# Kernel optimization log

Hardware: AMD Instinct MI355X
Metric: run time of the kernel (lower is better)

The kernel has to match this reference:

```python
import jax, jax.numpy as jnp
import numpy as np

MUL = 64          # multiplicity of 0e and 1o channels
N_NODES = 50000
N_EDGES = 800000
NUM_NEIGHBORS = 16.0
SILU_NORM = 1.679177  # e3nn normalize2mom constant for silu


def setup_inputs() -> dict:
    key = jax.random.key(0)
    ks = jax.random.split(key, 9)
    node_in = jax.random.normal(ks[0], (N_NODES, 4 * MUL), dtype=jnp.float32)  # 64x0e + 64x1o
    edge_src = jax.random.randint(ks[1], (N_EDGES,), 0, N_NODES)
    edge_dst = jax.random.randint(ks[2], (N_EDGES,), 0, N_NODES)
    edge_attr = jax.random.normal(ks[3], (N_EDGES, 4), dtype=jnp.float32)      # 1x0e + 1x1o
    edge_len_emb = jax.random.uniform(ks[4], (N_EDGES, 10), dtype=jnp.float32)
    # tensor-product path weights [mul_in, mul_out] (mul_edge = 1)
    w_00_0 = jax.random.normal(ks[5], (MUL, MUL), dtype=jnp.float32)  # 0e x 0e -> 0e
    w_11_0 = jax.random.normal(ks[6], (MUL, MUL), dtype=jnp.float32)  # 1o x 1o -> 0e
    w_01_1 = jax.random.normal(ks[7], (MUL, MUL), dtype=jnp.float32)  # 0e x 1o -> 1o
    w_10_1 = jax.random.normal(ks[8], (MUL, MUL), dtype=jnp.float32)  # 1o x 0e -> 1o
    kf = jax.random.split(jax.random.fold_in(key, 1), 2)
    fc_w1 = jax.random.normal(kf[0], (10, 64), dtype=jnp.float32)
    fc_w2 = jax.random.normal(kf[1], (64, 1), dtype=jnp.float32)
    return {"node_in": node_in, "edge_attr": edge_attr, "edge_len_emb": edge_len_emb,
            "w_00_0": w_00_0, "w_11_0": w_11_0, "w_01_1": w_01_1, "w_10_1": w_10_1,
            "fc_w1": fc_w1, "fc_w2": fc_w2, "edge_src": edge_src, "edge_dst": edge_dst}


def reference(node_in, edge_attr, edge_len_emb, w_00_0, w_11_0, w_01_1, w_10_1,
              fc_w1, fc_w2, edge_src, edge_dst):
    # gather source node features per edge
    src = node_in[edge_src]                      # [E, 256]
    s0 = src[:, :MUL]                            # [E, mul]       scalars 0e
    s1 = src[:, MUL:].reshape(-1, MUL, 3)        # [E, mul, 3]    vectors 1o
    a0 = edge_attr[:, 0:1]                       # [E, 1]   edge 0e
    a1 = edge_attr[:, 1:4]                       # [E, 3]   edge 1o

    # fully-connected tensor product: path norm 1/sqrt(num_paths * fan_in)
    alpha = np.float32(1.0 / np.sqrt(2.0 * MUL))
    inv_sqrt3 = np.float32(1.0 / np.sqrt(3.0))
    # scalar output: 0e x 0e -> 0e  and  1o . 1o -> 0e (CG = delta/sqrt(3))
    out0 = alpha * (jnp.einsum('ei,io->eo', s0 * a0, w_00_0)
                    + inv_sqrt3 * jnp.einsum('eim,em,io->eo', s1, a1, w_11_0))   # [E, mul]
    # vector output: 0e x 1o -> 1o  and  1o x 0e -> 1o (CG = identity)
    out1 = alpha * (jnp.einsum('ei,io,em->eom', s0, w_01_1, a1)
                    + jnp.einsum('eim,io->eom', s1 * a0[:, :, None], w_10_1))     # [E, mul, 3]
    msg_ang = jnp.concatenate([out0, out1.reshape(-1, 3 * MUL)], axis=1)         # [E, 256]

    # radial MLP gate: FullyConnectedNet([10, 64, 1], silu)
    h = jax.nn.silu(edge_len_emb @ fc_w1 / np.float32(np.sqrt(10.0))) * np.float32(SILU_NORM)
    msg_rad = h @ fc_w2 / np.float32(np.sqrt(64.0))                              # [E, 1]

    messages = msg_ang * msg_rad
    agg = jax.ops.segment_sum(messages, edge_dst, num_segments=node_in.shape[0])
    return agg / np.float32(np.sqrt(NUM_NEIGHBORS))
```

## Files before the change

kernel.cpp:

```cpp
#include <hip/hip_runtime.h>

#define NE 800000
#define NN 50000
#define MAXD 56
#define FILL_BLK (NE / 256)
#define XC_BLK (NN / 8)

typedef __attribute__((ext_vector_type(4))) unsigned short ushort4v;
typedef __attribute__((ext_vector_type(8))) unsigned short ushort8;
typedef __attribute__((ext_vector_type(4))) _Float16 f16x4;
typedef __attribute__((ext_vector_type(4))) float f32x4;

static constexpr float ALPHA      = 0.08838834764831845f;
static constexpr float INV3       = 0.57735026918962576f;
static constexpr float INV_SQRT10 = 0.31622776601683794f;
static constexpr float SILU_NORM  = 1.679177f;
static constexpr float QSCALE     = ALPHA * 0.25f;

__device__ __forceinline__ unsigned short f2h_bits(float f) {
  _Float16 h = (_Float16)f;
  unsigned short b;
  __builtin_memcpy(&b, &h, 2);
  return b;
}
__device__ __forceinline__ float h2f_bits(unsigned int b) {
  unsigned short s = (unsigned short)b;
  _Float16 h;
  __builtin_memcpy(&h, &s, 2);
  return (float)h;
}
__device__ __forceinline__ unsigned int packh2(float lo, float hi) {
  return (unsigned int)f2h_bits(lo) | ((unsigned int)f2h_bits(hi) << 16);
}

__global__ __launch_bounds__(256) void k_combo(
    const float* __restrict__ X, unsigned short* __restrict__ Xp,
    const float* __restrict__ attr, const float* __restrict__ emb,
    const float* __restrict__ w1, const float* __restrict__ w2,
    const int* __restrict__ esrc, const int* __restrict__ edst,
    int* __restrict__ cur, uint4* __restrict__ ell) {
  __shared__ float lds[2816];
  if (blockIdx.x < FILL_BLK) {
    int eb = blockIdx.x * 256;
    int e = eb + threadIdx.x;
    int dst = edst[e];
    int src = esrc[e];
    float4 a = *(const float4*)(attr + (size_t)e * 4);
    int slot = atomicAdd(&cur[dst], 1);

    const float* ebase = emb + (size_t)eb * 10;
#pragma unroll
    for (int j = 0; j < 10; j++)
      lds[j * 256 + threadIdx.x] = ebase[j * 256 + threadIdx.x];
    __syncthreads();
    const float* x = lds + threadIdx.x * 10;
    float r = 0.f;
#pragma unroll
    for (int j = 0; j < 64; j++) {
      float d = 0.f;
#pragma unroll
      for (int k = 0; k < 10; k++) d = fmaf(x[k], w1[k * 64 + j], d);
      d *= INV_SQRT10;
      float h = d * __builtin_amdgcn_rcpf(1.f + __expf(-d)) * SILU_NORM;
      r = fmaf(h, w2[j], r);
    }
    r *= 0.125f * QSCALE;
    if (slot < MAXD) {
      ell[(size_t)dst * MAXD + slot] =
          make_uint4((unsigned)src, packh2(r * a.x, r * a.y),
                     packh2(r * a.z, r * a.w), 0u);
    }
  } else {
    int n0 = (blockIdx.x - FILL_BLK) * 8;
    const float4* Xs = (const float4*)(X + (size_t)n0 * 256);
    float4* L4 = (float4*)lds;
    L4[threadIdx.x] = Xs[threadIdx.x];
    L4[256 + threadIdx.x] = Xs[256 + threadIdx.x];
    __syncthreads();
    int o = threadIdx.x & 63;
    int nl = threadIdx.x >> 6;
#pragma unroll
    for (int ii = 0; ii < 2; ii++) {
      int n_l = nl + ii * 4;
      const float* row = lds + n_l * 256;
      ushort4v v;
      v[0] = f2h_bits(row[o]);
      v[1] = f2h_bits(row[64 + 3 * o]);
      v[2] = f2h_bits(row[64 + 3 * o + 1]);
      v[3] = f2h_bits(row[64 + 3 * o + 2]);
      *(ushort4v*)(Xp + (size_t)(n0 + n_l) * 256 + o * 4) = v;
    }
  }
}

__device__ __forceinline__ void eop2(unsigned int q01, unsigned int q23,
                                     ushort8 y, float& u0a, float& u1a,
                                     float& v0a, float& v1a, float& v2a,
                                     float& w0a, float& w1a, float& w2a,
                                     float& u0b, float& u1b, float& v0b,
                                     float& v1b, float& v2b, float& w0b,
                                     float& w1b, float& w2b) {
  float q0 = h2f_bits(q01), q1 = h2f_bits(q01 >> 16);
  float q2 = h2f_bits(q23), q3 = h2f_bits(q23 >> 16);
  float x0 = h2f_bits(y[0]), xa = h2f_bits(y[1]);
  float xb = h2f_bits(y[2]), xc = h2f_bits(y[3]);
  u0a = fmaf(q0, x0, u0a);
  u1a = fmaf(q1, xa, u1a);
  u1a = fmaf(q2, xb, u1a);
  u1a = fmaf(q3, xc, u1a);
  v0a = fmaf(q1, x0, v0a);
  v1a = fmaf(q2, x0, v1a);
  v2a = fmaf(q3, x0, v2a);
  w0a = fmaf(q0, xa, w0a);
  w1a = fmaf(q0, xb, w1a);
  w2a = fmaf(q0, xc, w2a);
  float z0 = h2f_bits(y[4]), za = h2f_bits(y[5]);
  float zb = h2f_bits(y[6]), zc = h2f_bits(y[7]);
  u0b = fmaf(q0, z0, u0b);
  u1b = fmaf(q1, za, u1b);
  u1b = fmaf(q2, zb, u1b);
  u1b = fmaf(q3, zc, u1b);
  v0b = fmaf(q1, z0, v0b);
  v1b = fmaf(q2, z0, v1b);
  v2b = fmaf(q3, z0, v2b);
  w0b = fmaf(q0, za, w0b);
  w1b = fmaf(q0, zb, w1b);
  w2b = fmaf(q0, zc, w2b);
}

__global__ __launch_bounds__(256) void k_agg(
    const int* __restrict__ cur, const uint4* __restrict__ ell,
    const unsigned short* __restrict__ Xp, unsigned short* __restrict__ P) {
  int n = blockIdx.x * 4 + (threadIdx.x >> 6);
  int l = threadIdx.x & 63;
  int half = l >> 5;
  int lp = l & 31;
  int d = cur[n];
  if (d > MAXD) d = MAXD;
  const uint4* base = ell + (size_t)n * MAXD;

  float u0a = 0.f, u1a = 0.f, v0a = 0.f, v1a = 0.f, v2a = 0.f;
  float w0a = 0.f, w1a = 0.f, w2a = 0.f;
  float u0b = 0.f, u1b = 0.f, v0b = 0.f, v1b = 0.f, v2b = 0.f;
  float w0b = 0.f, w1b = 0.f, w2b = 0.f;

  int np = (d + 1) >> 1;
  int i = 0;
  for (; i + 4 <= np; i += 4) {
    uint4 rec[4];
    ushort8 y[4];
#pragma unroll
    for (int q = 0; q < 4; q++) {
      int idx = 2 * (i + q) + half;
      int cidx = idx < d ? idx : d - 1;
      rec[q] = base[cidx];
      if (idx >= d) {
        rec[q].y = 0u;
        rec[q].z = 0u;
      }
    }
#pragma unroll
    for (int q = 0; q < 4; q++)
      y[q] = *(const ushort8*)(Xp + ((size_t)rec[q].x << 8) + (lp << 3));
#pragma unroll
    for (int q = 0; q < 4; q++)
      eop2(rec[q].y, rec[q].z, y[q], u0a, u1a, v0a, v1a, v2a, w0a, w1a, w2a,
           u0b, u1b, v0b, v1b, v2b, w0b, w1b, w2b);
  }
  for (; i < np; i++) {
    int idx = 2 * i + half;
    int cidx = idx < d ? idx : d - 1;
    uint4 rec = base[cidx];
    if (idx >= d) {
      rec.y = 0u;
      rec.z = 0u;
    }
    ushort8 y = *(const ushort8*)(Xp + ((size_t)rec.x << 8) + (lp << 3));
    eop2(rec.y, rec.z, y, u0a, u1a, v0a, v1a, v2a, w0a, w1a, w2a, u0b, u1b,
         v0b, v1b, v2b, w0b, w1b, w2b);
  }

  u0a += __shfl_xor(u0a, 32, 64);
  u1a += __shfl_xor(u1a, 32, 64);
  v0a += __shfl_xor(v0a, 32, 64);
  v1a += __shfl_xor(v1a, 32, 64);
  v2a += __shfl_xor(v2a, 32, 64);
  w0a += __shfl_xor(w0a, 32, 64);
  w1a += __shfl_xor(w1a, 32, 64);
  w2a += __shfl_xor(w2a, 32, 64);
  u0b += __shfl_xor(u0b, 32, 64);
  u1b += __shfl_xor(u1b, 32, 64);
  v0b += __shfl_xor(v0b, 32, 64);
  v1b += __shfl_xor(v1b, 32, 64);
  v2b += __shfl_xor(v2b, 32, 64);
  w0b += __shfl_xor(w0b, 32, 64);
  w1b += __shfl_xor(w1b, 32, 64);
  w2b += __shfl_xor(w2b, 32, 64);

  size_t pb = (size_t)n * 512;
  int om = 2 * lp + half;
  P[pb + 0 * 64 + om] = f2h_bits(half ? u0b : u0a);
  P[pb + 1 * 64 + om] = f2h_bits((half ? u1b : u1a) * INV3);
  P[pb + 2 * 64 + om] = f2h_bits(half ? v0b : v0a);
  P[pb + 3 * 64 + om] = f2h_bits(half ? v1b : v1a);
  P[pb + 4 * 64 + om] = f2h_bits(half ? v2b : v2a);
  P[pb + 5 * 64 + om] = f2h_bits(half ? w0b : w0a);
  P[pb + 6 * 64 + om] = f2h_bits(half ? w1b : w1a);
  P[pb + 7 * 64 + om] = f2h_bits(half ? w2b : w2a);
}

__global__ __launch_bounds__(256) void k_post(
    const unsigned short* __restrict__ P, const float* __restrict__ W00,
    const float* __restrict__ W11, const float* __restrict__ W01,
    const float* __restrict__ W10, float* __restrict__ out) {
  int l = threadIdx.x & 63;
  int lr = l & 15, lq = l >> 4;
  int tile = blockIdx.x * 4 + (threadIdx.x >> 6);
  int nb = tile * 16;
  if (nb >= NN) return;

  f16x4 a[8][4];
  const unsigned short* Pb = P + (size_t)(nb + lr) * 512;
#pragma unroll
  for (int c = 0; c < 8; c++) {
#pragma unroll
    for (int kq = 0; kq < 4; kq++) {
      ushort4v t = *(const ushort4v*)(Pb + c * 64 + kq * 16 + lq * 4);
      f16x4 af;
      __builtin_memcpy(&af, &t, 8);
      a[c][kq] = af;
    }
  }

#pragma unroll
  for (int j = 0; j < 4; j++) {
    int col = 16 * j + lr;
    f16x4 b00[4], b11[4], b01[4], b10[4];
#pragma unroll
    for (int kq = 0; kq < 4; kq++) {
#pragma unroll
      for (int i = 0; i < 4; i++) {
        int row = kq * 16 + lq * 4 + i;
        b00[kq][i] = (_Float16)W00[row * 64 + col];
        b11[kq][i] = (_Float16)W11[row * 64 + col];
        b01[kq][i] = (_Float16)W01[row * 64 + col];
        b10[kq][i] = (_Float16)W10[row * 64 + col];
      }
    }
    f32x4 acc0 = {0.f, 0.f, 0.f, 0.f};
#pragma unroll
    for (int kq = 0; kq < 4; kq++) {
      acc0 = __builtin_amdgcn_mfma_f32_16x16x16f16(a[0][kq], b00[kq], acc0, 0,
                                                   0, 0);
      acc0 = __builtin_amdgcn_mfma_f32_16x16x16f16(a[1][kq], b11[kq], acc0, 0,
                                                   0, 0);
    }
#pragma unroll
    for (int r = 0; r < 4; r++)
      out[(size_t)(nb + lq * 4 + r) * 256 + col] = acc0[r];
#pragma unroll
    for (int m = 0; m < 3; m++) {
      f32x4 acc = {0.f, 0.f, 0.f, 0.f};
#pragma unroll
      for (int kq = 0; kq < 4; kq++) {
        acc = __builtin_amdgcn_mfma_f32_16x16x16f16(a[2 + m][kq], b01[kq], acc,
                                                    0, 0, 0);
        acc = __builtin_amdgcn_mfma_f32_16x16x16f16(a[5 + m][kq], b10[kq], acc,
                                                    0, 0, 0);
      }
#pragma unroll
      for (int r = 0; r < 4; r++)
        out[(size_t)(nb + lq * 4 + r) * 256 + 64 + 3 * col + m] = acc[r];
    }
  }
}

extern "C" void kernel_launch(void* const* d_in, const int* in_sizes, int n_in,
                              void* d_out, int out_size, void* d_ws,
                              size_t ws_size, hipStream_t stream) {
  const float* node_in = (const float*)d_in[0];
  const float* edge_attr = (const float*)d_in[1];
  const float* emb = (const float*)d_in[2];
  const float* w00 = (const float*)d_in[3];
  const float* w11 = (const float*)d_in[4];
  const float* w01 = (const float*)d_in[5];
  const float* w10 = (const float*)d_in[6];
  const float* fw1 = (const float*)d_in[7];
  const float* fw2 = (const float*)d_in[8];
  const int* esrc = (const int*)d_in[9];
  const int* edst = (const int*)d_in[10];
  float* out = (float*)d_out;

  char* ws = (char*)d_ws;
  unsigned short* Xp = (unsigned short*)ws; ws += (size_t)NN * 256 * 2;
  uint4* ell = (uint4*)ws;                  ws += (size_t)NN * MAXD * 16;
  unsigned short* P = (unsigned short*)ws;  ws += (size_t)NN * 512 * 2;
  int* cur = (int*)ws;                      ws += (size_t)NN * 4;

  (void)hipMemsetAsync(cur, 0, (size_t)NN * 4, stream);
  k_combo<<<FILL_BLK + XC_BLK, 256, 0, stream>>>(
      node_in, Xp, edge_attr, emb, fw1, fw2, esrc, edst, cur, ell);
  k_agg<<<NN / 4, 256, 0, stream>>>(cur, ell, Xp, P);
  k_post<<<(NN / 16 + 3) / 4, 256, 0, stream>>>(P, w00, w11, w01, w10, out);
}
```

Measured before the change: 160.4 us.

## Compute radial MLP gate with fp16 MFMA instead of scalar loops

The per-edge radial MLP (10x64 matmul, SiLU, 64->1 reduction) in the fill kernel is now computed with 16x16x16 fp16 MFMA instructions on a zero-padded LDS tile. A shuffle reduction and a select tree then produce one gate value per edge. This targets the scalar FMA and exp work of 64 hidden units per thread, but it adds LDS zeroing, an extra barrier, shuffles, and fp16 rounding of the embeddings and weights.

```diff
diff --git a/kernel.cpp b/kernel.cpp
--- a/kernel.cpp
+++ b/kernel.cpp
@@ -39,32 +39,103 @@
     const float* __restrict__ w1, const float* __restrict__ w2,
     const int* __restrict__ esrc, const int* __restrict__ edst,
     int* __restrict__ cur, uint4* __restrict__ ell) {
-  __shared__ float lds[2816];
+  __shared__ float lds[4096 + 256];
+  int tid = threadIdx.x;
   if (blockIdx.x < FILL_BLK) {
     int eb = blockIdx.x * 256;
-    int e = eb + threadIdx.x;
+    int e = eb + tid;
     int dst = edst[e];
     int src = esrc[e];
     float4 a = *(const float4*)(attr + (size_t)e * 4);
     int slot = atomicAdd(&cur[dst], 1);
 
+    float4* z4 = (float4*)lds;
+    z4[tid] = make_float4(0.f, 0.f, 0.f, 0.f);
+    z4[tid + 256] = make_float4(0.f, 0.f, 0.f, 0.f);
+    z4[tid + 512] = make_float4(0.f, 0.f, 0.f, 0.f);
+    z4[tid + 768] = make_float4(0.f, 0.f, 0.f, 0.f);
+    __syncthreads();
     const float* ebase = emb + (size_t)eb * 10;
 #pragma unroll
-    for (int j = 0; j < 10; j++)
-      lds[j * 256 + threadIdx.x] = ebase[j * 256 + threadIdx.x];
+    for (int j = 0; j < 10; j++) {
+      int flat = j * 256 + tid;
+      float v = ebase[flat];
+      int edge = flat / 10;
+      int k = flat - edge * 10;
+      lds[edge * 16 + k] = v;
+    }
     __syncthreads();
-    const float* x = lds + threadIdx.x * 10;
-    float r = 0.f;
-#pragma unroll
-    for (int j = 0; j < 64; j++) {
-      float d = 0.f;
-#pragma unroll
-      for (int k = 0; k < 10; k++) d = fmaf(x[k], w1[k * 64 + j], d);
-      d *= INV_SQRT10;
-      float h = d * __builtin_amdgcn_rcpf(1.f + __expf(-d)) * SILU_NORM;
-      r = fmaf(h, w2[j], r);
-    }
-    r *= 0.125f * QSCALE;
+
+    int w = tid >> 6, l = tid & 63;
+    int lr = l & 15, q = l >> 4;
+
+    f16x4 af[4];
+#pragma unroll
+    for (int mt = 0; mt < 4; mt++) {
+      f32x4 t = *(const f32x4*)(lds + (w * 64 + mt * 16 + lr) * 16 + q * 4);
+#pragma unroll
+      for (int i = 0; i < 4; i++) af[mt][i] = (_Float16)(t[i] * INV_SQRT10);
+    }
+    f16x4 bf[4];
+#pragma unroll
+    for (int nt = 0; nt < 4; nt++) {
+#pragma unroll
+      for (int i = 0; i < 4; i++) {
+        int k = q * 4 + i;
+        bf[nt][i] = (k < 10) ? (_Float16)w1[k * 64 + nt * 16 + lr]
+                             : (_Float16)0.f;
+      }
+    }
+
+    float s[4][4];
+#pragma unroll
+    for (int mt = 0; mt < 4; mt++)
+#pragma unroll
+      for (int r = 0; r < 4; r++) s[mt][r] = 0.f;
+
+#pragma unroll
+    for (int nt = 0; nt < 4; nt++) {
+      float w2s = w2[nt * 16 + lr] * SILU_NORM;
+#pragma unroll
+      for (int mt = 0; mt < 4; mt++) {
+        f32x4 acc = {0.f, 0.f, 0.f, 0.f};
+        acc = __builtin_amdgcn_mfma_f32_16x16x16f16(af[mt], bf[nt], acc, 0, 0,
+                                                    0);
+#pragma unroll
+        for (int r = 0; r < 4; r++) {
+          float dv = acc[r];
+          float sg = __builtin_amdgcn_rcpf(1.f + __expf(-dv));
+          s[mt][r] = fmaf(dv * sg, w2s, s[mt][r]);
+        }
+      }
+    }
+
+#pragma unroll
+    for (int mt = 0; mt < 4; mt++)
+#pragma unroll
+      for (int r = 0; r < 4; r++) {
+        float v = s[mt][r];
+        v += __shfl_xor(v, 1, 64);
+        v += __shfl_xor(v, 2, 64);
+        v += __shfl_xor(v, 4, 64);
+        v += __shfl_xor(v, 8, 64);
+        s[mt][r] = v;
+      }
+
+    int b0 = lr & 1, b1 = lr & 2, b2 = lr & 4, b3 = lr & 8;
+    float a00 = b0 ? s[0][1] : s[0][0], a01 = b0 ? s[0][3] : s[0][2];
+    float a10 = b0 ? s[1][1] : s[1][0], a11 = b0 ? s[1][3] : s[1][2];
+    float a20 = b0 ? s[2][1] : s[2][0], a21 = b0 ? s[2][3] : s[2][2];
+    float a30 = b0 ? s[3][1] : s[3][0], a31 = b0 ? s[3][3] : s[3][2];
+    float c0 = b1 ? a01 : a00, c1 = b1 ? a11 : a10;
+    float c2 = b1 ? a21 : a20, c3 = b1 ? a31 : a30;
+    float d0 = b2 ? c1 : c0, d1 = b2 ? c3 : c2;
+    float val = b3 ? d1 : d0;
+    float* sE = lds + 4096;
+    sE[w * 64 + (lr >> 2) * 16 + q * 4 + (lr & 3)] = val;
+    __syncthreads();
+
+    float r = sE[tid] * 0.125f * QSCALE;
     if (slot < MAXD) {
       ell[(size_t)dst * MAXD + slot] =
           make_uint4((unsigned)src, packh2(r * a.x, r * a.y),
@@ -74,11 +145,11 @@
     int n0 = (blockIdx.x - FILL_BLK) * 8;
     const float4* Xs = (const float4*)(X + (size_t)n0 * 256);
     float4* L4 = (float4*)lds;
-    L4[threadIdx.x] = Xs[threadIdx.x];
-    L4[256 + threadIdx.x] = Xs[256 + threadIdx.x];
+    L4[tid] = Xs[tid];
+    L4[256 + tid] = Xs[256 + tid];
     __syncthreads();
-    int o = threadIdx.x & 63;
-    int nl = threadIdx.x >> 6;
+    int o = tid & 63;
+    int nl = tid >> 6;
 #pragma unroll
     for (int ii = 0; ii < 2; ii++) {
       int n_l = nl + ii * 4;
```

After: 165.7 us. 1.03x slower.
